# Kernel optimization log

Hardware: AMD Instinct MI355X
Metric: run time of the kernel (lower is better)

## Reference

```python
import jax, jax.numpy as jnp
import numpy as np

D = 512; H = 8; DH = D // H; NB = 4; DMLP = 2048; L = 32; ROPE_DIM = 32
SCALE = DH ** -0.25  # scale_exponent = -0.25, applied to both q and k
EPS = 1e-6


def _rms(x, g):
    return x * jax.lax.rsqrt(jnp.mean(x * x, axis=-1, keepdims=True) + EPS) * g


def _rope_tables(T):
    inv = 1.0 / (10000.0 ** (jnp.arange(0, ROPE_DIM, 2, dtype=jnp.float32) / ROPE_DIM))
    ang = jnp.arange(T, dtype=jnp.float32)[:, None] * inv[None, :]  # (T, ROPE_DIM/2)
    return jnp.cos(ang), jnp.sin(ang)


def _apply_rope(x, cos, sin):
    # x: (N, H, T, DH); rotate first ROPE_DIM dims, interleaved pairs
    xr, rest = x[..., :ROPE_DIM], x[..., ROPE_DIM:]
    x1, x2 = xr[..., 0::2], xr[..., 1::2]
    c = cos[None, None]; s = sin[None, None]
    r1 = x1 * c - x2 * s
    r2 = x1 * s + x2 * c
    rot = jnp.stack([r1, r2], axis=-1).reshape(xr.shape)
    return jnp.concatenate([rot, rest], axis=-1)


def _mha(q_in, kv_in, wq, wk, bk, wv, wo, rope=None):
    # q_in: (N, Lq, D), kv_in: (N, Lk, D); k has bias, q/v/o do not
    N, Lq, _ = q_in.shape
    Lk = kv_in.shape[1]
    q = (q_in @ wq).reshape(N, Lq, H, DH).transpose(0, 2, 1, 3)
    k = (kv_in @ wk + bk).reshape(N, Lk, H, DH).transpose(0, 2, 1, 3)
    v = (kv_in @ wv).reshape(N, Lk, H, DH).transpose(0, 2, 1, 3)
    if rope is not None:
        cos, sin = rope
        q = _apply_rope(q, cos, sin)
        k = _apply_rope(k, cos, sin)
    scores = jnp.einsum('nhqd,nhkd->nhqk', q * SCALE, k * SCALE)
    a = jax.nn.softmax(scores, axis=-1)
    o = jnp.einsum('nhqk,nhkd->nhqd', a, v).transpose(0, 2, 1, 3).reshape(N, Lq, D)
    return o @ wo


def _geglu_mlp(x, w1, w2):
    h = x @ w1                       # (..., 2*DMLP)
    a, g = jnp.split(h, 2, axis=-1)
    return (a * jax.nn.gelu(g)) @ w2


def setup_inputs() -> dict:
    key = jax.random.key(0)
    ks = jax.random.split(key, 16)
    w = lambda k, shape: jax.random.normal(k, shape, dtype=jnp.float32) * 0.02
    B, T, C = 8, 128, 64
    return {
        'source': jax.random.normal(ks[0], (B * T, C, D), dtype=jnp.float32),
        'query_latents': jax.random.normal(ks[1], (L, D), dtype=jnp.float32),
        'ca_ln': jnp.ones((NB, 3, D), jnp.float32),
        'ca_wq': w(ks[2], (NB, D, D)), 'ca_wk': w(ks[3], (NB, D, D)),
        'ca_bk': jnp.zeros((NB, D), jnp.float32),
        'ca_wv': w(ks[4], (NB, D, D)), 'ca_wo': w(ks[5], (NB, D, D)),
        'ca_w1': w(ks[6], (NB, D, 2 * DMLP)), 'ca_w2': w(ks[7], (NB, DMLP, D)),
        'ta_ln': jnp.ones((NB, 2, D), jnp.float32),
        'ta_wq': w(ks[8], (NB, D, D)), 'ta_wk': w(ks[9], (NB, D, D)),
        'ta_bk': jnp.zeros((NB, D), jnp.float32),
        'ta_wv': w(ks[10], (NB, D, D)), 'ta_wo': w(ks[11], (NB, D, D)),
        'ta_w1': w(ks[12], (NB, D, 2 * DMLP)), 'ta_w2': w(ks[13], (NB, DMLP, D)),
        'B': B, 'T': T,
    }


def reference(source, query_latents, ca_ln, ca_wq, ca_wk, ca_bk, ca_wv, ca_wo,
              ca_w1, ca_w2, ta_ln, ta_wq, ta_wk, ta_bk, ta_wv, ta_wo, ta_w1,
              ta_w2, B, T):
    BT = source.shape[0]
    rope = _rope_tables(T)
    latents = jnp.broadcast_to(query_latents[None], (BT, L, D))
    for b in range(NB):
        # --- PerceiverResamplerBlock (spatial cross-attn) ---
        l_n = _rms(latents, ca_ln[b, 0])
        s_n = _rms(source, ca_ln[b, 1])
        kv = jnp.concatenate([s_n, l_n], axis=1)  # (BT, C+L, D)
        latents = latents + _mha(l_n, kv, ca_wq[b], ca_wk[b], ca_bk[b], ca_wv[b], ca_wo[b])
        latents = latents + _geglu_mlp(_rms(latents, ca_ln[b, 2]), ca_w1[b], ca_w2[b])
        # --- TemporalAttentionBlock: (B T) L D -> (B L) T D ---
        x = latents.reshape(B, T, L, D).transpose(0, 2, 1, 3).reshape(B * L, T, D)
        x_n = _rms(x, ta_ln[b, 0])
        x = x + _mha(x_n, x_n, ta_wq[b], ta_wk[b], ta_bk[b], ta_wv[b], ta_wo[b], rope=rope)
        x = x + _geglu_mlp(_rms(x, ta_ln[b, 1]), ta_w1[b], ta_w2[b])
        latents = x.reshape(B, L, T, D).transpose(0, 2, 1, 3).reshape(BT, L, D)
    # '(B T) L D -> B T (L D)'
    return latents.reshape(B, T, L * D)
```

## Files before the change

kernel.cpp:

```cpp
#include <hip/hip_runtime.h>
#include <stdint.h>


typedef short    bf16x8 __attribute__((ext_vector_type(8)));
typedef float    f32x4  __attribute__((ext_vector_type(4)));
typedef uint16_t u16;

__device__ __forceinline__ float bf2f(uint32_t u) {
  union { uint32_t i; float f; } x; x.i = u << 16; return x.f;
}
__device__ __forceinline__ u16 f2bf(float f) {
  union { float f; uint32_t i; } x; x.f = f;
  return (u16)((x.i + 0x7fffu + ((x.i >> 16) & 1u)) >> 16);
}
__device__ __forceinline__ float gelu_t(float x) {
  float u = 0.7978845608028654f * (x + 0.044715f * x * x * x);
  float t = 1.f - 2.f / (__expf(2.f * u) + 1.f);
  return 0.5f * x * (1.f + t);
}
template<int RMAP>
__device__ __forceinline__ int maprow(int r) {
  if (RMAP == 0) return r;
  int b = r >> 12, rem = r & 4095;
  return ((b << 7) + (rem & 127)) * 32 + (rem >> 7);
}
__device__ __forceinline__ void glds16(const u16* g, u16* l) {
  __builtin_amdgcn_global_load_lds((const __attribute__((address_space(1))) uint32_t*)(g),
                                   (__attribute__((address_space(3))) uint32_t*)(l),
                                   16, 0, 0);
}
__device__ __forceinline__ void kt_gate() {
  asm volatile("s_waitcnt vmcnt(0)" ::: "memory");
  __builtin_amdgcn_s_barrier();
  asm volatile("" ::: "memory");
}

__global__ __launch_bounds__(256) void transpose_cast(const float* __restrict__ src,
                                                      u16* __restrict__ dst,
                                                      int R, int C, size_t zsD) {
  src += (size_t)blockIdx.z * R * C;
  dst += (size_t)blockIdx.z * zsD;
  __shared__ float t[32][33];
  int c0 = blockIdx.x * 32, r0 = blockIdx.y * 32;
  int tx = threadIdx.x & 31, ty = threadIdx.x >> 5;
#pragma unroll
  for (int i = 0; i < 32; i += 8) t[ty + i][tx] = src[(size_t)(r0 + ty + i) * C + c0 + tx];
  __syncthreads();
#pragma unroll
  for (int i = 0; i < 32; i += 8)
    dst[(size_t)(c0 + ty + i) * R + r0 + tx] = f2bf(t[tx][ty + i]);
}

__global__ __launch_bounds__(256) void transpose_w1(const float* __restrict__ src,
                                                    u16* __restrict__ dst) {
  src += (size_t)blockIdx.z * 512 * 4096;
  dst += (size_t)blockIdx.z * 512 * 4096;
  __shared__ float t[32][33];
  int c0 = blockIdx.x * 32, r0 = blockIdx.y * 32;
  int m0 = (c0 >> 8) * 128 + ((c0 >> 6) & 3) * 32 + ((c0 & 32) ? 2048 : 0);
  int tx = threadIdx.x & 31, ty = threadIdx.x >> 5;
#pragma unroll
  for (int i = 0; i < 32; i += 8) t[ty + i][tx] = src[(size_t)(r0 + ty + i) * 4096 + m0 + tx];
  __syncthreads();
#pragma unroll
  for (int i = 0; i < 32; i += 8)
    dst[(size_t)(c0 + ty + i) * 512 + r0 + tx] = f2bf(t[tx][ty + i]);
}

__global__ void rope_init(float* cosT, float* sinT) {
  int idx = blockIdx.x * 256 + threadIdx.x;
  if (idx < 128 * 16) {
    int t = idx >> 4, j = idx & 15;
    float inv = __expf(-logf(10000.f) * (float)j / 16.f);
    float a = (float)t * inv;
    cosT[idx] = cosf(a);
    sinT[idx] = sinf(a);
  }
}

__global__ __launch_bounds__(256) void init_lat(const float* __restrict__ ql,
                                                float* __restrict__ lat) {
  size_t i = (size_t)blockIdx.x * 256 + threadIdx.x;
  int r = (int)(i >> 7), cw = (int)(i & 127);
  int l = r & 31;
  ((float4*)lat)[i] = ((const float4*)ql)[l * 128 + cw];
}

template<int RMAP>
__global__ __launch_bounds__(256) void rms_rows(const float* __restrict__ src,
                                                const float* __restrict__ g,
                                                u16* __restrict__ out) {
  const int wid = threadIdx.x >> 6, lane = threadIdx.x & 63;
  const int row = (blockIdx.x << 2) + wid;
  const int srow = maprow<RMAP>(row);
  const float4* p = (const float4*)(src + (size_t)srow * 512);
  float4 v0 = p[lane * 2], v1 = p[lane * 2 + 1];
  float ss = v0.x * v0.x + v0.y * v0.y + v0.z * v0.z + v0.w * v0.w +
             v1.x * v1.x + v1.y * v1.y + v1.z * v1.z + v1.w * v1.w;
#pragma unroll
  for (int m = 1; m < 64; m <<= 1) ss += __shfl_xor(ss, m);
  const float rs = rsqrtf(ss * (1.f / 512.f) + 1e-6f);
  const float4* gp = (const float4*)g;
  float4 g0 = gp[lane * 2], g1 = gp[lane * 2 + 1];
  u16 rb[8];
  rb[0] = f2bf(v0.x * rs * g0.x); rb[1] = f2bf(v0.y * rs * g0.y);
  rb[2] = f2bf(v0.z * rs * g0.z); rb[3] = f2bf(v0.w * rs * g0.w);
  rb[4] = f2bf(v1.x * rs * g1.x); rb[5] = f2bf(v1.y * rs * g1.y);
  rb[6] = f2bf(v1.z * rs * g1.z); rb[7] = f2bf(v1.w * rs * g1.w);
  *(int4*)(out + (size_t)row * 512 + lane * 8) = *(int4*)rb;
}

template<int EPI, int RMAP, int AMAP>
__global__ __launch_bounds__(512, 2) void gemm256(const u16* __restrict__ A,
                                                  const u16* __restrict__ A2,
                                                  const u16* __restrict__ Bt,
                                                  u16* __restrict__ outH,
                                                  float* __restrict__ latF,
                                                  const float* __restrict__ bias,
                                                  int M, int N, int K, int nb) {
  __shared__ __align__(16) u16 Ab[2][256 * 64];
  __shared__ __align__(16) u16 Bb[2][256 * 64];
  const int tid = threadIdx.x;
  const int m0 = blockIdx.y << 8;
  const int n0 = blockIdx.x << 8;
  const int wid = tid >> 6, lane = tid & 63;
  const int wm = wid >> 2, wn = wid & 3;
  const int lr = lane & 15, lg = lane >> 4;
  const int rx = (lr & 7) << 3;

  auto stageA = [&](int bf, int kt, int h) {
#pragma unroll
    for (int i = 0; i < 2; ++i) {
      const int e = (i * 512 + tid) * 8;
      const int r = e >> 6;
      const int cs = (e & 63) ^ ((r & 7) << 3);
      const u16* src;
      if constexpr (AMAP == 0) {
        src = A + (size_t)(m0 + h * 128 + r) * K + kt * 64 + cs;
      } else {
        const int R = m0 + h * 128 + r;
        const int n_ = R / 96;
        const int j = R - n_ * 96;
        src = (j < 64) ? A  + ((size_t)((nb + n_) * 64 + j)) * 512 + kt * 64 + cs
                       : A2 + ((size_t)((nb + n_) * 32 + (j - 64))) * 512 + kt * 64 + cs;
      }
      glds16(src, &Ab[bf][h * 8192 + e]);
    }
  };
  auto stageB = [&](int bf, int kt, int h) {
#pragma unroll
    for (int i = 0; i < 2; ++i) {
      const int e = (i * 512 + tid) * 8;
      const int r = e >> 6;
      const int cs = (e & 63) ^ ((r & 7) << 3);
      glds16(Bt + (size_t)(n0 + h * 128 + r) * K + kt * 64 + cs, &Bb[bf][h * 8192 + e]);
    }
  };

  f32x4 acc[8][4];
#pragma unroll
  for (int i = 0; i < 8; ++i)
#pragma unroll
    for (int j = 0; j < 4; ++j) acc[i][j] = (f32x4){0.f, 0.f, 0.f, 0.f};

  stageA(0, 0, 0); stageA(0, 0, 1);
  stageB(0, 0, 0); stageB(0, 0, 1);
  kt_gate();

  const int nkt = K >> 6;
  for (int kt = 0; kt < nkt; ++kt) {
    const int bf = kt & 1;
    const u16* Abase = &Ab[bf][0];
    const u16* Bbase = &Bb[bf][0];
    const bool pf = (kt + 1 < nkt);
    bf16x8 bfr[2][4];
#pragma unroll
    for (int p = 0; p < 4; ++p) {
      if (p == 0 && pf) { stageA(bf ^ 1, kt + 1, 0); stageA(bf ^ 1, kt + 1, 1); }
      if (p == 1 && pf) { stageB(bf ^ 1, kt + 1, 0); stageB(bf ^ 1, kt + 1, 1); }
      if (p == 0) {
#pragma unroll
        for (int ks = 0; ks < 2; ++ks)
#pragma unroll
          for (int in = 0; in < 4; ++in) {
            const int rw = wn * 64 + in * 16 + lr;
            bfr[ks][in] = *(const bf16x8*)&Bbase[rw * 64 + ((ks * 32 + lg * 8) ^ rx)];
          }
      }
      bf16x8 afr[2][2];
#pragma unroll
      for (int d = 0; d < 2; ++d)
#pragma unroll
        for (int ks = 0; ks < 2; ++ks) {
          const int rw = wm * 128 + (p * 2 + d) * 16 + lr;
          afr[d][ks] = *(const bf16x8*)&Abase[rw * 64 + ((ks * 32 + lg * 8) ^ rx)];
        }
      __builtin_amdgcn_s_setprio(1);
#pragma unroll
      for (int d = 0; d < 2; ++d)
#pragma unroll
        for (int in = 0; in < 4; ++in)
#pragma unroll
          for (int ks = 0; ks < 2; ++ks)
            acc[p * 2 + d][in] = __builtin_amdgcn_mfma_f32_16x16x32_bf16(
                afr[d][ks], bfr[ks][in], acc[p * 2 + d][in], 0, 0, 0);
      __builtin_amdgcn_s_setprio(0);
      if (p == 3) {
        kt_gate();
      } else {
        __builtin_amdgcn_s_barrier();
      }
    }
  }

  if constexpr (EPI == 3) {
    const int t128 = n0 >> 1;
#pragma unroll
    for (int im = 0; im < 8; ++im)
#pragma unroll
      for (int in = 0; in < 2; ++in)
#pragma unroll
        for (int j = 0; j < 4; ++j) {
          const int row = m0 + wm * 128 + im * 16 + lg * 4 + j;
          const int hcol = t128 + wn * 32 + in * 16 + lr;
          outH[(size_t)row * 2048 + hcol] = f2bf(acc[im][in][j] * gelu_t(acc[im][in + 2][j]));
        }
  } else if constexpr (EPI == 2) {
#pragma unroll
    for (int im = 0; im < 8; ++im)
#pragma unroll
      for (int in = 0; in < 4; ++in) {
        const int col = n0 + wn * 64 + in * 16 + lr;
#pragma unroll
        for (int j = 0; j < 4; ++j) {
          const int row = m0 + wm * 128 + im * 16 + lg * 4 + j;
          const size_t rr = (size_t)maprow<RMAP>(row) * 512 + col;
          latF[rr] += acc[im][in][j];
        }
      }
  } else {
    float bv4[4];
    if constexpr (EPI == 1) {
#pragma unroll
      for (int in = 0; in < 4; ++in)
        bv4[in] = (n0 < 512) ? bias[n0 + wn * 64 + in * 16 + lr] : 0.f;
    }
#pragma unroll
    for (int im = 0; im < 8; ++im)
#pragma unroll
      for (int in = 0; in < 4; ++in) {
        const int col = n0 + wn * 64 + in * 16 + lr;
#pragma unroll
        for (int j = 0; j < 4; ++j) {
          const int row = m0 + wm * 128 + im * 16 + lg * 4 + j;
          float v = acc[im][in][j];
          if constexpr (EPI == 1) v += bv4[in];
          outH[(size_t)row * N + col] = f2bf(v);
        }
      }
  }
}

__global__ __launch_bounds__(256) void attn_ca(const u16* q,
                                               const u16* __restrict__ kv,
                                               u16* o, int nb) {
  union __align__(16) SM {
    struct { u16 Qs[32][72]; u16 Ks[96][72]; } qk;
    u16 Pb[32][104];
  };
  __shared__ SM sm;
  __shared__ __align__(16) u16 Vt[64][104];
  __shared__ float pmax[2][32];
  __shared__ float psum[2][32];
  const int nl = blockIdx.x, n = nb + nl, h = blockIdx.y, tid = threadIdx.x;

  {
    int r = tid >> 3, c = (tid & 7) * 8;
    *(int4*)&sm.qk.Qs[r][c] = *(const int4*)&q[((size_t)n * 32 + r) * 512 + h * 64 + c];
  }
#pragma unroll
  for (int i = 0; i < 3; ++i) {
    int idx = i * 256 + tid;
    int r = idx >> 3, c = (idx & 7) * 8;
    *(int4*)&sm.qk.Ks[r][c] = *(const int4*)&kv[((size_t)nl * 96 + r) * 1024 + h * 64 + c];
  }
#pragma unroll
  for (int i = 0; i < 3; ++i) {
    int idx = i * 256 + tid;
    int dg = idx / 96, t = idx - dg * 96;
    int4 pv = *(const int4*)&kv[((size_t)nl * 96 + t) * 1024 + 512 + h * 64 + dg * 8];
    const u16* pu = (const u16*)&pv;
#pragma unroll
    for (int e = 0; e < 8; ++e) Vt[dg * 8 + e][t] = pu[e];
  }
  __syncthreads();

  const int wid = tid >> 6, lane = tid & 63, lr = lane & 15, lg = lane >> 4;
  const int m0 = (wid & 1) * 16, wnq = wid >> 1, nbc = wnq * 48;

  f32x4 sa[3];
#pragma unroll
  for (int f = 0; f < 3; ++f) sa[f] = (f32x4){0.f, 0.f, 0.f, 0.f};
#pragma unroll
  for (int ks = 0; ks < 2; ++ks) {
    bf16x8 a = *(const bf16x8*)&sm.qk.Qs[m0 + lr][ks * 32 + lg * 8];
#pragma unroll
    for (int f = 0; f < 3; ++f) {
      bf16x8 bb = *(const bf16x8*)&sm.qk.Ks[nbc + f * 16 + lr][ks * 32 + lg * 8];
      sa[f] = __builtin_amdgcn_mfma_f32_16x16x32_bf16(a, bb, sa[f], 0, 0, 0);
    }
  }

#pragma unroll
  for (int j = 0; j < 4; ++j) {
    float m = fmaxf(fmaxf(sa[0][j], sa[1][j]), sa[2][j]);
    m = fmaxf(m, __shfl_xor(m, 1));
    m = fmaxf(m, __shfl_xor(m, 2));
    m = fmaxf(m, __shfl_xor(m, 4));
    m = fmaxf(m, __shfl_xor(m, 8));
    if (lr == 0) pmax[wnq][m0 + lg * 4 + j] = m;
  }
  __syncthreads();
#pragma unroll
  for (int j = 0; j < 4; ++j) {
    const int row = m0 + lg * 4 + j;
    const float m = fmaxf(pmax[0][row], pmax[1][row]);
    float s = 0.f;
#pragma unroll
    for (int f = 0; f < 3; ++f) {
      float p = __expf(0.125f * (sa[f][j] - m));
      sa[f][j] = p;
      s += p;
    }
    s += __shfl_xor(s, 1); s += __shfl_xor(s, 2); s += __shfl_xor(s, 4); s += __shfl_xor(s, 8);
    if (lr == 0) psum[wnq][row] = s;
  }
#pragma unroll
  for (int f = 0; f < 3; ++f)
#pragma unroll
    for (int j = 0; j < 4; ++j)
      sm.Pb[m0 + lg * 4 + j][nbc + f * 16 + lr] = f2bf(sa[f][j]);
  __syncthreads();

  const int n0d = wnq * 32;
  f32x4 oa[2];
#pragma unroll
  for (int f = 0; f < 2; ++f) oa[f] = (f32x4){0.f, 0.f, 0.f, 0.f};
#pragma unroll
  for (int ks = 0; ks < 3; ++ks) {
    bf16x8 a = *(const bf16x8*)&sm.Pb[m0 + lr][ks * 32 + lg * 8];
#pragma unroll
    for (int f = 0; f < 2; ++f) {
      bf16x8 bb = *(const bf16x8*)&Vt[n0d + f * 16 + lr][ks * 32 + lg * 8];
      oa[f] = __builtin_amdgcn_mfma_f32_16x16x32_bf16(a, bb, oa[f], 0, 0, 0);
    }
  }
#pragma unroll
  for (int j = 0; j < 4; ++j) {
    const int row = m0 + lg * 4 + j;
    const float inv = 1.f / (psum[0][row] + psum[1][row]);
#pragma unroll
    for (int f = 0; f < 2; ++f)
      o[((size_t)n * 32 + row) * 512 + h * 64 + n0d + f * 16 + lr] = f2bf(oa[f][j] * inv);
  }
}

__global__ __launch_bounds__(256) void attn_ta(const u16* q,
                                               const u16* __restrict__ kv,
                                               const float* __restrict__ cosT,
                                               const float* __restrict__ sinT,
                                               u16* o) {
  union __align__(16) SM {
    struct { u16 Qs[128][72]; u16 Ks[128][72]; } qk;
    u16 Pb[128][136];
  };
  __shared__ SM sm;
  __shared__ __align__(16) u16 Vt[64][136];
  __shared__ float pmax[2][128];
  __shared__ float psum[2][128];
  const int n = blockIdx.x, h = blockIdx.y, tid = threadIdx.x;

#pragma unroll
  for (int i = 0; i < 16; ++i) {
    int idx = i * 256 + tid;
    int t = idx >> 5, pr = idx & 31;
    uint32_t uq = *(const uint32_t*)&q[((size_t)n * 128 + t) * 512 + h * 64 + pr * 2];
    uint32_t uk = *(const uint32_t*)&kv[((size_t)n * 128 + t) * 1024 + h * 64 + pr * 2];
    float q1 = bf2f(uq & 0xffff), q2 = bf2f(uq >> 16);
    float k1 = bf2f(uk & 0xffff), k2 = bf2f(uk >> 16);
    if (pr < 16) {
      float c = cosT[t * 16 + pr], s = sinT[t * 16 + pr];
      float a;
      a = q1 * c - q2 * s; q2 = q1 * s + q2 * c; q1 = a;
      a = k1 * c - k2 * s; k2 = k1 * s + k2 * c; k1 = a;
    }
    sm.qk.Qs[t][pr * 2] = f2bf(q1); sm.qk.Qs[t][pr * 2 + 1] = f2bf(q2);
    sm.qk.Ks[t][pr * 2] = f2bf(k1); sm.qk.Ks[t][pr * 2 + 1] = f2bf(k2);
  }
#pragma unroll
  for (int i = 0; i < 4; ++i) {
    int idx = i * 256 + tid;
    int t = idx & 127, d0 = (idx >> 7) * 8;
    int4 pv = *(const int4*)&kv[((size_t)n * 128 + t) * 1024 + 512 + h * 64 + d0];
    const u16* pu = (const u16*)&pv;
#pragma unroll
    for (int e = 0; e < 8; ++e) Vt[d0 + e][t] = pu[e];
  }
  __syncthreads();

  const int wid = tid >> 6, lane = tid & 63, lr = lane & 15, lg = lane >> 4;
  const int wm = wid >> 1, wn = wid & 1;
  const int rbase = wm * 64;

  f32x4 sa[4][4];
#pragma unroll
  for (int i = 0; i < 4; ++i)
#pragma unroll
    for (int j = 0; j < 4; ++j) sa[i][j] = (f32x4){0.f, 0.f, 0.f, 0.f};
#pragma unroll
  for (int ks = 0; ks < 2; ++ks) {
    bf16x8 av[4], bv[4];
#pragma unroll
    for (int im = 0; im < 4; ++im)
      av[im] = *(const bf16x8*)&sm.qk.Qs[rbase + im * 16 + lr][ks * 32 + lg * 8];
#pragma unroll
    for (int in = 0; in < 4; ++in)
      bv[in] = *(const bf16x8*)&sm.qk.Ks[wn * 64 + in * 16 + lr][ks * 32 + lg * 8];
#pragma unroll
    for (int im = 0; im < 4; ++im)
#pragma unroll
      for (int in = 0; in < 4; ++in)
        sa[im][in] = __builtin_amdgcn_mfma_f32_16x16x32_bf16(av[im], bv[in], sa[im][in], 0, 0, 0);
  }

#pragma unroll
  for (int im = 0; im < 4; ++im)
#pragma unroll
    for (int j = 0; j < 4; ++j) {
      float m = fmaxf(fmaxf(sa[im][0][j], sa[im][1][j]), fmaxf(sa[im][2][j], sa[im][3][j]));
      m = fmaxf(m, __shfl_xor(m, 1));
      m = fmaxf(m, __shfl_xor(m, 2));
      m = fmaxf(m, __shfl_xor(m, 4));
      m = fmaxf(m, __shfl_xor(m, 8));
      if (lr == 0) pmax[wn][rbase + im * 16 + lg * 4 + j] = m;
    }
  __syncthreads();
#pragma unroll
  for (int im = 0; im < 4; ++im)
#pragma unroll
    for (int j = 0; j < 4; ++j) {
      const int row = rbase + im * 16 + lg * 4 + j;
      const float m = fmaxf(pmax[0][row], pmax[1][row]);
      float s = 0.f;
#pragma unroll
      for (int in = 0; in < 4; ++in) {
        float p = __expf(0.125f * (sa[im][in][j] - m));
        sa[im][in][j] = p;
        s += p;
      }
      s += __shfl_xor(s, 1); s += __shfl_xor(s, 2); s += __shfl_xor(s, 4); s += __shfl_xor(s, 8);
      if (lr == 0) psum[wn][row] = s;
    }
#pragma unroll
  for (int im = 0; im < 4; ++im)
#pragma unroll
    for (int in = 0; in < 4; ++in)
#pragma unroll
      for (int j = 0; j < 4; ++j)
        sm.Pb[rbase + im * 16 + lg * 4 + j][wn * 64 + in * 16 + lr] = f2bf(sa[im][in][j]);
  __syncthreads();

  f32x4 oa[2][4];
#pragma unroll
  for (int i = 0; i < 2; ++i)
#pragma unroll
    for (int j = 0; j < 4; ++j) oa[i][j] = (f32x4){0.f, 0.f, 0.f, 0.f};
#pragma unroll
  for (int ks = 0; ks < 4; ++ks) {
    bf16x8 av[2], bv[4];
#pragma unroll
    for (int im = 0; im < 2; ++im)
      av[im] = *(const bf16x8*)&sm.Pb[wid * 32 + im * 16 + lr][ks * 32 + lg * 8];
#pragma unroll
    for (int in = 0; in < 4; ++in)
      bv[in] = *(const bf16x8*)&Vt[in * 16 + lr][ks * 32 + lg * 8];
#pragma unroll
    for (int im = 0; im < 2; ++im)
#pragma unroll
      for (int in = 0; in < 4; ++in)
        oa[im][in] = __builtin_amdgcn_mfma_f32_16x16x32_bf16(av[im], bv[in], oa[im][in], 0, 0, 0);
  }
#pragma unroll
  for (int im = 0; im < 2; ++im)
#pragma unroll
    for (int j = 0; j < 4; ++j) {
      const int qi = wid * 32 + im * 16 + lg * 4 + j;
      const float inv = 1.f / (psum[0][qi] + psum[1][qi]);
#pragma unroll
      for (int in = 0; in < 4; ++in)
        o[((size_t)n * 128 + qi) * 512 + h * 64 + in * 16 + lr] = f2bf(oa[im][in][j] * inv);
    }
}

extern "C" void kernel_launch(void* const* d_in, const int* in_sizes, int n_in,
                              void* d_out, int out_size, void* d_ws, size_t ws_size,
                              hipStream_t stream) {
  const float* source = (const float*)d_in[0];
  const float* qlat   = (const float*)d_in[1];
  const float* ca_ln  = (const float*)d_in[2];
  const float* ca_wq  = (const float*)d_in[3];
  const float* ca_wk  = (const float*)d_in[4];
  const float* ca_bk  = (const float*)d_in[5];
  const float* ca_wv  = (const float*)d_in[6];
  const float* ca_wo  = (const float*)d_in[7];
  const float* ca_w1  = (const float*)d_in[8];
  const float* ca_w2  = (const float*)d_in[9];
  const float* ta_ln  = (const float*)d_in[10];
  const float* ta_wq  = (const float*)d_in[11];
  const float* ta_wk  = (const float*)d_in[12];
  const float* ta_bk  = (const float*)d_in[13];
  const float* ta_wv  = (const float*)d_in[14];
  const float* ta_wo  = (const float*)d_in[15];
  const float* ta_w1  = (const float*)d_in[16];
  const float* ta_w2  = (const float*)d_in[17];
  float* lat = (float*)d_out;
  char* ws = (char*)d_ws;
  (void)in_sizes; (void)n_in; (void)out_size;

  if (ws_size < 251674624ull) return;

  const size_t WQ = 512 * 512, W1SZ = (size_t)512 * 4096, W2SZ = (size_t)2048 * 512;
  const size_t O_CA_WQ = 0,
               O_CA_KV = 4 * WQ,
               O_CA_WO = 12 * WQ,
               O_CA_W1 = 16 * WQ,
               O_CA_W2 = O_CA_W1 + 4 * W1SZ,
               O_TA_WQ = O_CA_W2 + 4 * W2SZ,
               O_TA_KV = O_TA_WQ + 4 * WQ,
               O_TA_WO = O_TA_KV + 8 * WQ,
               O_TA_W1 = O_TA_WO + 4 * WQ,
               O_TA_W2 = O_TA_W1 + 4 * W1SZ;

  u16*   W    = (u16*)ws;
  u16*   xn   = (u16*)(ws + 67108864);
  u16*   shat = (u16*)(ws + 100663296);
  u16*   qb   = (u16*)(ws + 167772160);
  u16*   kvb  = (u16*)(ws + 201326592);
  u16*   h2   = shat;
  u16*   takv = shat;
  float* cosT = (float*)(ws + 251658240);
  float* sinT = (float*)(ws + 251666432);

  transpose_cast<<<dim3(16, 16, 4), 256, 0, stream>>>(ca_wq, W + O_CA_WQ, 512, 512, WQ);
  transpose_cast<<<dim3(16, 16, 4), 256, 0, stream>>>(ca_wk, W + O_CA_KV, 512, 512, 2 * WQ);
  transpose_cast<<<dim3(16, 16, 4), 256, 0, stream>>>(ca_wv, W + O_CA_KV + WQ, 512, 512, 2 * WQ);
  transpose_cast<<<dim3(16, 16, 4), 256, 0, stream>>>(ca_wo, W + O_CA_WO, 512, 512, WQ);
  transpose_w1 <<<dim3(128, 16, 4), 256, 0, stream>>>(ca_w1, W + O_CA_W1);
  transpose_cast<<<dim3(16, 64, 4), 256, 0, stream>>>(ca_w2, W + O_CA_W2, 2048, 512, W2SZ);
  transpose_cast<<<dim3(16, 16, 4), 256, 0, stream>>>(ta_wq, W + O_TA_WQ, 512, 512, WQ);
  transpose_cast<<<dim3(16, 16, 4), 256, 0, stream>>>(ta_wk, W + O_TA_KV, 512, 512, 2 * WQ);
  transpose_cast<<<dim3(16, 16, 4), 256, 0, stream>>>(ta_wv, W + O_TA_KV + WQ, 512, 512, 2 * WQ);
  transpose_cast<<<dim3(16, 16, 4), 256, 0, stream>>>(ta_wo, W + O_TA_WO, 512, 512, WQ);
  transpose_w1 <<<dim3(128, 16, 4), 256, 0, stream>>>(ta_w1, W + O_TA_W1);
  transpose_cast<<<dim3(16, 64, 4), 256, 0, stream>>>(ta_w2, W + O_TA_W2, 2048, 512, W2SZ);
  rope_init<<<8, 256, 0, stream>>>(cosT, sinT);
  init_lat<<<16384, 256, 0, stream>>>(qlat, lat);

  for (int b = 0; b < 4; ++b) {
    const u16* wqt   = W + O_CA_WQ + (size_t)b * WQ;
    const u16* wkvt  = W + O_CA_KV + (size_t)b * 2 * WQ;
    const u16* wot   = W + O_CA_WO + (size_t)b * WQ;
    const u16* w1t   = W + O_CA_W1 + (size_t)b * W1SZ;
    const u16* w2t   = W + O_CA_W2 + (size_t)b * W2SZ;
    const u16* twqt  = W + O_TA_WQ + (size_t)b * WQ;
    const u16* twkvt = W + O_TA_KV + (size_t)b * 2 * WQ;
    const u16* twot  = W + O_TA_WO + (size_t)b * WQ;
    const u16* tw1t  = W + O_TA_W1 + (size_t)b * W1SZ;
    const u16* tw2t  = W + O_TA_W2 + (size_t)b * W2SZ;

    rms_rows<0><<<8192, 256, 0, stream>>>(lat, ca_ln + b * 1536, xn);
    rms_rows<0><<<16384, 256, 0, stream>>>(source, ca_ln + b * 1536 + 512, shat);
    gemm256<0, 0, 0><<<dim3(2, 128), 512, 0, stream>>>(xn, nullptr, wqt, qb, nullptr, nullptr, 32768, 512, 512, 0);
    for (int c = 0; c < 4; ++c) {
      gemm256<1, 0, 1><<<dim3(4, 96), 512, 0, stream>>>(shat, xn, wkvt, kvb, nullptr, ca_bk + b * 512, 24576, 1024, 512, c * 256);
      attn_ca<<<dim3(256, 8), 256, 0, stream>>>(qb, kvb, qb, c * 256);
    }
    gemm256<2, 0, 0><<<dim3(2, 128), 512, 0, stream>>>(qb, nullptr, wot, nullptr, lat, nullptr, 32768, 512, 512, 0);
    rms_rows<0><<<8192, 256, 0, stream>>>(lat, ca_ln + b * 1536 + 1024, xn);
    gemm256<3, 0, 0><<<dim3(16, 128), 512, 0, stream>>>(xn, nullptr, w1t, h2, nullptr, nullptr, 32768, 4096, 512, 0);
    gemm256<2, 0, 0><<<dim3(2, 128), 512, 0, stream>>>(h2, nullptr, w2t, nullptr, lat, nullptr, 32768, 512, 2048, 0);

    rms_rows<1><<<8192, 256, 0, stream>>>(lat, ta_ln + b * 1024, xn);
    gemm256<0, 0, 0><<<dim3(2, 128), 512, 0, stream>>>(xn, nullptr, twqt, qb, nullptr, nullptr, 32768, 512, 512, 0);
    gemm256<1, 0, 0><<<dim3(4, 128), 512, 0, stream>>>(xn, nullptr, twkvt, takv, nullptr, ta_bk + b * 512, 32768, 1024, 512, 0);
    attn_ta<<<dim3(256, 8), 256, 0, stream>>>(qb, takv, cosT, sinT, qb);
    gemm256<2, 1, 0><<<dim3(2, 128), 512, 0, stream>>>(qb, nullptr, twot, nullptr, lat, nullptr, 32768, 512, 512, 0);
    rms_rows<1><<<8192, 256, 0, stream>>>(lat, ta_ln + b * 1024 + 512, xn);
    gemm256<3, 0, 0><<<dim3(16, 128), 512, 0, stream>>>(xn, nullptr, tw1t, h2, nullptr, nullptr, 32768, 4096, 512, 0);
    gemm256<2, 1, 0><<<dim3(2, 128), 512, 0, stream>>>(h2, nullptr, tw2t, nullptr, lat, nullptr, 32768, 512, 2048, 0);
  }
}
```

Before: 5.313 ms.

## Triple-buffer A tiles with partial vmcnt waits and remap workgroup order

The GEMM now keeps three LDS buffers for the A operand and prefetches A two k-steps ahead while B stays double-buffered. End-of-iteration waits use vmcnt(4) instead of draining every outstanding load, so loads can overlap across iterations. Workgroup IDs are also permuted in strides of eight, likely to spread neighbouring tiles across XCDs/L2. The extra A buffer raises LDS use to 160KB per block, which may cut occupancy below the two blocks per CU requested by launch bounds, and the vmcnt counting has to exactly match the number of loads issued.

New measurement: 5.045 ms. -5.0%, faster.

```diff
diff --git a/kernel.cpp b/kernel.cpp
--- a/kernel.cpp
+++ b/kernel.cpp
@@ -28,11 +28,6 @@
   __builtin_amdgcn_global_load_lds((const __attribute__((address_space(1))) uint32_t*)(g),
                                    (__attribute__((address_space(3))) uint32_t*)(l),
                                    16, 0, 0);
-}
-__device__ __forceinline__ void kt_gate() {
-  asm volatile("s_waitcnt vmcnt(0)" ::: "memory");
-  __builtin_amdgcn_s_barrier();
-  asm volatile("" ::: "memory");
 }
 
 __global__ __launch_bounds__(256) void transpose_cast(const float* __restrict__ src,
@@ -118,42 +113,45 @@
                                                   float* __restrict__ latF,
                                                   const float* __restrict__ bias,
                                                   int M, int N, int K, int nb) {
-  __shared__ __align__(16) u16 Ab[2][256 * 64];
+  __shared__ __align__(16) u16 Ab[3][256 * 64];
   __shared__ __align__(16) u16 Bb[2][256 * 64];
   const int tid = threadIdx.x;
-  const int m0 = blockIdx.y << 8;
-  const int n0 = blockIdx.x << 8;
+  const int nwg = gridDim.x * gridDim.y;
+  int bid = blockIdx.y * gridDim.x + blockIdx.x;
+  bid = (bid & 7) * (nwg >> 3) + (bid >> 3);
+  const int m0 = (bid / gridDim.x) << 8;
+  const int n0 = (bid % gridDim.x) << 8;
   const int wid = tid >> 6, lane = tid & 63;
   const int wm = wid >> 2, wn = wid & 3;
   const int lr = lane & 15, lg = lane >> 4;
   const int rx = (lr & 7) << 3;
 
-  auto stageA = [&](int bf, int kt, int h) {
-#pragma unroll
-    for (int i = 0; i < 2; ++i) {
+  auto stageA = [&](int slot, int kt) {
+#pragma unroll
+    for (int i = 0; i < 4; ++i) {
       const int e = (i * 512 + tid) * 8;
       const int r = e >> 6;
       const int cs = (e & 63) ^ ((r & 7) << 3);
       const u16* src;
       if constexpr (AMAP == 0) {
-        src = A + (size_t)(m0 + h * 128 + r) * K + kt * 64 + cs;
+        src = A + (size_t)(m0 + r) * K + kt * 64 + cs;
       } else {
-        const int R = m0 + h * 128 + r;
+        const int R = m0 + r;
         const int n_ = R / 96;
         const int j = R - n_ * 96;
         src = (j < 64) ? A  + ((size_t)((nb + n_) * 64 + j)) * 512 + kt * 64 + cs
                        : A2 + ((size_t)((nb + n_) * 32 + (j - 64))) * 512 + kt * 64 + cs;
       }
-      glds16(src, &Ab[bf][h * 8192 + e]);
+      glds16(src, &Ab[slot][e]);
     }
   };
-  auto stageB = [&](int bf, int kt, int h) {
-#pragma unroll
-    for (int i = 0; i < 2; ++i) {
+  auto stageB = [&](int slot, int kt) {
+#pragma unroll
+    for (int i = 0; i < 4; ++i) {
       const int e = (i * 512 + tid) * 8;
       const int r = e >> 6;
       const int cs = (e & 63) ^ ((r & 7) << 3);
-      glds16(Bt + (size_t)(n0 + h * 128 + r) * K + kt * 64 + cs, &Bb[bf][h * 8192 + e]);
+      glds16(Bt + (size_t)(n0 + r) * K + kt * 64 + cs, &Bb[slot][e]);
     }
   };
 
@@ -163,21 +161,24 @@
 #pragma unroll
     for (int j = 0; j < 4; ++j) acc[i][j] = (f32x4){0.f, 0.f, 0.f, 0.f};
 
-  stageA(0, 0, 0); stageA(0, 0, 1);
-  stageB(0, 0, 0); stageB(0, 0, 1);
-  kt_gate();
+  stageA(0, 0);
+  stageB(0, 0);
+  stageA(1, 1);
+  asm volatile("s_waitcnt vmcnt(4)" ::: "memory");
+  __builtin_amdgcn_s_barrier();
+  asm volatile("" ::: "memory");
 
   const int nkt = K >> 6;
+  int sl0 = 0;
+  int sl2 = 2;
   for (int kt = 0; kt < nkt; ++kt) {
-    const int bf = kt & 1;
-    const u16* Abase = &Ab[bf][0];
-    const u16* Bbase = &Bb[bf][0];
-    const bool pf = (kt + 1 < nkt);
+    const u16* Abase = &Ab[sl0][0];
+    const u16* Bbase = &Bb[kt & 1][0];
     bf16x8 bfr[2][4];
 #pragma unroll
     for (int p = 0; p < 4; ++p) {
-      if (p == 0 && pf) { stageA(bf ^ 1, kt + 1, 0); stageA(bf ^ 1, kt + 1, 1); }
-      if (p == 1 && pf) { stageB(bf ^ 1, kt + 1, 0); stageB(bf ^ 1, kt + 1, 1); }
+      if (p == 0 && kt + 1 < nkt) stageB((kt + 1) & 1, kt + 1);
+      if (p == 1 && kt + 2 < nkt) stageA(sl2, kt + 2);
       if (p == 0) {
 #pragma unroll
         for (int ks = 0; ks < 2; ++ks)
@@ -206,11 +207,18 @@
                 afr[d][ks], bfr[ks][in], acc[p * 2 + d][in], 0, 0, 0);
       __builtin_amdgcn_s_setprio(0);
       if (p == 3) {
-        kt_gate();
+        if (kt + 1 < nkt) {
+          if (kt + 2 < nkt) asm volatile("s_waitcnt vmcnt(4)" ::: "memory");
+          else              asm volatile("s_waitcnt vmcnt(0)" ::: "memory");
+          __builtin_amdgcn_s_barrier();
+          asm volatile("" ::: "memory");
+        }
       } else {
         __builtin_amdgcn_s_barrier();
       }
     }
+    sl0 = (sl0 == 2) ? 0 : sl0 + 1;
+    sl2 = (sl2 == 2) ? 0 : sl2 + 1;
   }
 
   if constexpr (EPI == 3) {
```
